# Kernel tuning notes

Measured on AMD Instinct MI355X. Metric: run time of the kernel, lower is better.

Reference implementation:

```python
import math
import jax, jax.numpy as jnp
import numpy as np

D_MODEL = 1024
N_HEAD = 16
HEAD_DIM = D_MODEL // N_HEAD
THETA = 10000.0


def precompute_rope(seq_len, head_dim):
    half = head_dim // 2
    inv_freq = 1.0 / (THETA ** (jnp.arange(half, dtype=jnp.float32) / half))
    pos = jnp.arange(seq_len, dtype=jnp.float32)
    freqs = jnp.outer(pos, inv_freq)  # [S, half]
    return jnp.cos(freqs), jnp.sin(freqs)


def apply_rope(x, cos, sin):
    # x: [B, H, S, Dh]; cos/sin: [S, Dh//2] -> broadcast over B, H
    x_even = x[..., 0::2]
    x_odd = x[..., 1::2]
    cos = cos[None, None]
    sin = sin[None, None]
    out_even = x_even * cos - x_odd * sin
    out_odd = x_even * sin + x_odd * cos
    # interleave back: stack on last axis then flatten pairs
    return jnp.stack((out_even, out_odd), axis=-1).reshape(x.shape)


def setup_inputs() -> dict:
    key = jax.random.key(0)
    kx, kq, kp = jax.random.split(key, 3)
    x = jax.random.normal(kx, (4, 2048, D_MODEL), dtype=jnp.float32)
    s = 1.0 / math.sqrt(D_MODEL)
    # torch Linear weight is [out, in]; we store transposed [in, out] for x @ W
    W_qkv = jax.random.normal(kq, (D_MODEL, 3 * D_MODEL), dtype=jnp.float32) * s
    W_proj = jax.random.normal(kp, (D_MODEL, D_MODEL), dtype=jnp.float32) * s
    return {"x": x, "W_qkv": W_qkv, "W_proj": W_proj}


def reference(x, W_qkv, W_proj):
    bsz, seqlen, d_model = x.shape
    qkv = x @ W_qkv  # [B, S, 3D]
    q, k, v = jnp.split(qkv, 3, axis=-1)
    def to_heads(t):
        return t.reshape(bsz, seqlen, N_HEAD, HEAD_DIM).transpose(0, 2, 1, 3)
    q, k, v = to_heads(q), to_heads(k), to_heads(v)  # [B, H, S, Dh]
    cos, sin = precompute_rope(seqlen, HEAD_DIM)
    q = apply_rope(q, cos, sin)
    k = apply_rope(k, cos, sin)
    att = jnp.einsum('bhqd,bhkd->bhqk', q, k) * (1.0 / math.sqrt(HEAD_DIM))
    causal = jnp.tril(jnp.ones((seqlen, seqlen), dtype=bool))
    att = jnp.where(causal[None, None], att, -jnp.inf)
    att = jax.nn.softmax(att, axis=-1)
    y = jnp.einsum('bhqk,bhkd->bhqd', att, v)
    y = y.transpose(0, 2, 1, 3).reshape(bsz, seqlen, d_model)
    return y @ W_proj
```

## Files before the change

### kernel.cpp

```cpp
#include <hip/hip_runtime.h>


#define BATCH 4
#define SEQ   2048
#define DM    1024
#define NH    16
#define HD    64
#define QKV_W 3072

typedef short bf16x8 __attribute__((ext_vector_type(8)));
typedef float f32x4  __attribute__((ext_vector_type(4)));
typedef unsigned u32x4 __attribute__((ext_vector_type(4)));
typedef unsigned short bf16_t;

__device__ __forceinline__ unsigned short f2bf(float f) {
  unsigned u = __float_as_uint(f);
  u += 0x7fffu + ((u >> 16) & 1u);
  return (unsigned short)(u >> 16);
}
__device__ __forceinline__ float bf2f(unsigned short s) {
  return __uint_as_float((unsigned)s << 16);
}
__device__ __forceinline__ void gld16(const void* g, void* l) {
  __builtin_amdgcn_global_load_lds(
      (const __attribute__((address_space(1))) unsigned int*)g,
      (__attribute__((address_space(3))) unsigned int*)l, 16, 0, 0);
}
__device__ __forceinline__ unsigned cvt_pk_bf16(float a, float b) {
  unsigned r;
  asm("v_cvt_pk_bf16_f32 %0, %1, %2" : "=v"(r) : "v"(a), "v"(b));
  return r;
}
__device__ __forceinline__ void permlane32_swap(unsigned& a, unsigned& b) {
  asm("v_permlane32_swap_b32 %0, %1" : "+v"(a), "+v"(b));
}
__device__ __forceinline__ void permlane16_swap(unsigned& a, unsigned& b) {
  asm("v_permlane16_swap_b32 %0, %1" : "+v"(a), "+v"(b));
}

__global__ __launch_bounds__(256) void k_transpose(const float* __restrict__ W,
                                                   bf16_t* __restrict__ Wt,
                                                   int K, int N) {
  __shared__ float tile[32][33];
  const int tx = threadIdx.x, ty = threadIdx.y;
  const int n0 = blockIdx.x * 32, k0 = blockIdx.y * 32;
#pragma unroll
  for (int j = 0; j < 4; ++j)
    tile[ty + j * 8][tx] = W[(size_t)(k0 + ty + j * 8) * N + n0 + tx];
  __syncthreads();
#pragma unroll
  for (int j = 0; j < 4; ++j)
    Wt[(size_t)(n0 + ty + j * 8) * K + k0 + tx] = f2bf(tile[tx][ty + j * 8]);
}

__global__ __launch_bounds__(256) void k_cvt(const float* __restrict__ x,
                                             bf16_t* __restrict__ xb) {
  const int i = (blockIdx.x * 256 + threadIdx.x) * 4;
  float4 v = *(const float4*)(x + i);
  unsigned lo = (unsigned)f2bf(v.x) | ((unsigned)f2bf(v.y) << 16);
  unsigned hi = (unsigned)f2bf(v.z) | ((unsigned)f2bf(v.w) << 16);
  *(uint2*)(xb + i) = make_uint2(lo, hi);
}

__global__ __launch_bounds__(256) void k_rope(bf16_t* __restrict__ qkv) {
  const int t = blockIdx.x * 256 + threadIdx.x;
  const int i = t & 31;
  const int h = (t >> 5) & 15;
  const int s = (t >> 9) & 2047;
  const int b = t >> 20;
  const float inv = __expf((float)i * -0.28782313662425575f);
  float sn, cs;
  sincosf((float)s * inv, &sn, &cs);
  size_t base = ((size_t)(b * SEQ + s)) * QKV_W + h * HD + 2 * i;
#pragma unroll
  for (int part = 0; part < 2; ++part) {
    unsigned u = *(unsigned*)(qkv + base + part * DM);
    float e = bf2f((unsigned short)(u & 0xffffu));
    float o = bf2f((unsigned short)(u >> 16));
    unsigned short e2 = f2bf(e * cs - o * sn);
    unsigned short o2 = f2bf(e * sn + o * cs);
    *(unsigned*)(qkv + base + part * DM) = (unsigned)e2 | ((unsigned)o2 << 16);
  }
}

template<int MODE>
__global__ __launch_bounds__(256) void k_gemm(const bf16_t* __restrict__ A,
                                              const bf16_t* __restrict__ Bt,
                                              void* __restrict__ Cout,
                                              bf16_t* __restrict__ vt,
                                              int M, int N, int K) {
  __shared__ __align__(16) short As[128 * 64];
  __shared__ __align__(16) short Bs[128 * 64];
  const int tid = threadIdx.x;
  const int wave = tid >> 6, lane = tid & 63;
  const int quad = lane >> 4, l16 = lane & 15;
  const int wm = (wave >> 1) * 64, wn = (wave & 1) * 64;
  const int bm = blockIdx.y * 128, bn = blockIdx.x * 128;

  f32x4 acc[4][4];
#pragma unroll
  for (int i = 0; i < 4; ++i)
#pragma unroll
    for (int j = 0; j < 4; ++j) acc[i][j] = f32x4{0.f, 0.f, 0.f, 0.f};

  const int srow = tid >> 3;
  const int sg   = (tid & 7) ^ (srow & 7);
  const bf16_t* Ap = A  + (size_t)(bm + srow) * K + sg * 8;
  const bf16_t* Bp = Bt + (size_t)(bn + srow) * K + sg * 8;
  short* Ad = As + tid * 8;
  short* Bd = Bs + tid * 8;

  for (int k0 = 0; k0 < K; k0 += 64) {
    __syncthreads();
#pragma unroll
    for (int pp = 0; pp < 4; ++pp) {
      gld16(Ap + (size_t)(pp * 32) * K + k0, Ad + pp * 2048);
      gld16(Bp + (size_t)(pp * 32) * K + k0, Bd + pp * 2048);
    }
    __syncthreads();
#pragma unroll
    for (int ks = 0; ks < 2; ++ks) {
      bf16x8 af[4], bfr[4];
#pragma unroll
      for (int i = 0; i < 4; ++i)
        af[i] = *(const bf16x8*)&As[(wm + i * 16 + l16) * 64 +
                                    (((ks * 4 + quad) ^ (l16 & 7)) << 3)];
#pragma unroll
      for (int j = 0; j < 4; ++j)
        bfr[j] = *(const bf16x8*)&Bs[(wn + j * 16 + l16) * 64 +
                                     (((ks * 4 + quad) ^ (l16 & 7)) << 3)];
#pragma unroll
      for (int i = 0; i < 4; ++i)
#pragma unroll
        for (int j = 0; j < 4; ++j)
          acc[i][j] = __builtin_amdgcn_mfma_f32_16x16x32_bf16(af[i], bfr[j], acc[i][j], 0, 0, 0);
    }
  }
#pragma unroll
  for (int i = 0; i < 4; ++i)
#pragma unroll
    for (int j = 0; j < 4; ++j) {
      const int col = bn + wn + j * 16 + l16;
      const int row0 = bm + wm + i * 16 + quad * 4;
      if (MODE == 1 && col >= 2048) {
        const int d = col - 2048;
        const int hh = d >> 6, dd = d & 63;
        const int bb = row0 >> 11, ss = row0 & 2047;
        ushort4 pk;
        pk.x = f2bf(acc[i][j][0]); pk.y = f2bf(acc[i][j][1]);
        pk.z = f2bf(acc[i][j][2]); pk.w = f2bf(acc[i][j][3]);
        *(ushort4*)(vt + ((size_t)((bb * NH + hh) * HD + dd)) * SEQ + ss) = pk;
      } else {
#pragma unroll
        for (int r = 0; r < 4; ++r) {
          if (MODE == 1)
            ((bf16_t*)Cout)[(size_t)(row0 + r) * N + col] = f2bf(acc[i][j][r]);
          else
            ((float*)Cout)[(size_t)(row0 + r) * N + col] = acc[i][j][r];
        }
      }
    }
}

__global__ __launch_bounds__(512, 2) void k_gqkv(const bf16_t* __restrict__ A,
                                                 const bf16_t* __restrict__ Bt,
                                                 bf16_t* __restrict__ qkv,
                                                 bf16_t* __restrict__ vt) {
  const int K = 1024;
  __shared__ __align__(16) short LA[2 * 2 * 4096];
  __shared__ __align__(16) short LB[2 * 2 * 12288];
  const int tid = threadIdx.x;
  const int lane = tid & 63, wave = tid >> 6;
  const int quad = lane >> 4, l16 = lane & 15;
  const int ah = wave >> 2;
  const int wn4 = wave & 3;

  int bid = (int)blockIdx.x;
  bid = (bid & 7) * 64 + (bid >> 3);
  const int bm = (bid >> 3) * 128, bn = (bid & 7) * 384;

  f32x4 acc[4][6];
#pragma unroll
  for (int i = 0; i < 4; ++i)
#pragma unroll
    for (int j = 0; j < 6; ++j) acc[i][j] = f32x4{0.f, 0.f, 0.f, 0.f};

  const int sg = (tid & 3) ^ ((tid >> 2) & 3) ^ ((tid >> 4) & 3);
  const bf16_t* aS = A  + (size_t)(bm + (tid >> 2)) * K + sg * 8;
  const bf16_t* bS = Bt + (size_t)(bn + (tid >> 2)) * K + sg * 8;
  short* dA = LA + tid * 8;
  short* dB = LB + tid * 8;

  const int g = quad ^ (l16 & 3) ^ ((l16 >> 2) & 3);
  const int abase = (ah * 64 + l16) * 32 + g * 8;
  const int bbase = (wn4 * 96 + l16) * 32 + g * 8;

#define WAITV(n) asm volatile("s_waitcnt vmcnt(" n ")" ::: "memory")
#define STGR(kts, kss)                                                         \
  do {                                                                         \
    const size_t kc_ = (size_t)((kts) * 64 + (kss) * 32);                      \
    const int rb_ = ((kts) & 1) * 2 + (kss);                                   \
    gld16(aS + kc_, dA + rb_ * 4096);                                          \
    gld16(bS + kc_, dB + rb_ * 12288);                                         \
    gld16(bS + (size_t)128 * 1024 + kc_, dB + rb_ * 12288 + 4096);             \
    gld16(bS + (size_t)256 * 1024 + kc_, dB + rb_ * 12288 + 8192);             \
  } while (0)
#define PHASE(kt, ks, STAGE_STMT, WAIT_STMT)                                   \
  do {                                                                         \
    const short* la_ = LA + (((kt) & 1) * 2 + (ks)) * 4096 + abase;            \
    const short* lb_ = LB + (((kt) & 1) * 2 + (ks)) * 12288 + bbase;           \
    bf16x8 af[4], bfr[6];                                                      \
    _Pragma("unroll") for (int mi = 0; mi < 4; ++mi)                           \
        af[mi] = *(const bf16x8*)(la_ + mi * 512);                             \
    _Pragma("unroll") for (int nj = 0; nj < 6; ++nj)                           \
        bfr[nj] = *(const bf16x8*)(lb_ + nj * 512);                            \
    STAGE_STMT;                                                                \
    WAIT_STMT;                                                                 \
    __builtin_amdgcn_s_barrier();                                              \
    __builtin_amdgcn_s_setprio(1);                                             \
    _Pragma("unroll") for (int mi = 0; mi < 4; ++mi)                           \
      _Pragma("unroll") for (int nj = 0; nj < 6; ++nj)                         \
        acc[mi][nj] = __builtin_amdgcn_mfma_f32_16x16x32_bf16(                 \
            af[mi], bfr[nj], acc[mi][nj], 0, 0, 0);                            \
    __builtin_amdgcn_s_setprio(0);                                             \
    asm volatile("s_waitcnt lgkmcnt(0)" ::: "memory");                         \
    __builtin_amdgcn_s_barrier();                                              \
  } while (0)

  STGR(0, 0); STGR(0, 1); STGR(1, 0);
  WAITV("8");
  __builtin_amdgcn_s_barrier();

#pragma unroll 1
  for (int ph = 0; ph < 29; ++ph) {
    const int kt = ph >> 1, ks = ph & 1;
    const int pk = ph + 3;
    PHASE(kt, ks, STGR(pk >> 1, pk & 1), WAITV("8"));
  }
  PHASE(14, 1, (void)0, WAITV("4"));
  PHASE(15, 0, (void)0, WAITV("0"));
  PHASE(15, 1, (void)0, (void)0);

#pragma unroll
  for (int mi = 0; mi < 4; ++mi)
#pragma unroll
    for (int nj = 0; nj < 6; ++nj) {
      const int col = bn + wn4 * 96 + nj * 16 + l16;
      const int row0 = bm + ah * 64 + mi * 16 + quad * 4;
      if (col >= 2048) {
        const int d = col - 2048;
        const int hh = d >> 6, dd = d & 63;
        const int bb = row0 >> 11, ss = row0 & 2047;
        ushort4 pk;
        pk.x = f2bf(acc[mi][nj][0]); pk.y = f2bf(acc[mi][nj][1]);
        pk.z = f2bf(acc[mi][nj][2]); pk.w = f2bf(acc[mi][nj][3]);
        *(ushort4*)(vt + ((size_t)((bb * NH + hh) * HD + dd)) * SEQ + ss) = pk;
      } else {
#pragma unroll
        for (int r = 0; r < 4; ++r)
          qkv[(size_t)(row0 + r) * QKV_W + col] = f2bf(acc[mi][nj][r]);
      }
    }
#undef WAITV
#undef STGR
#undef PHASE
}

#define QSCALE 0.18033688011112042f
__global__ __launch_bounds__(256, 2) void k_attn(const bf16_t* __restrict__ qkv,
                                                 const bf16_t* __restrict__ vt,
                                                 bf16_t* __restrict__ y) {
  __shared__ __align__(16) short KV[2][4][64 * 32];
  const int tid = threadIdx.x;
  const int lane = tid & 63;
  const int quad = lane >> 4, l16 = lane & 15;
  const int wave = tid >> 6;
  const int l = blockIdx.x;
  const int p = (l >> 3) & 7;
  const int g = ((l >> 6) << 3) | (l & 7);
  const int h = g & 15, b = g >> 4;
  const size_t bbase = (size_t)b * SEQ * QKV_W;
  const int srow = tid >> 2;
  const int sc8  = (tid & 3) * 8;
  const bf16_t* kbase = qkv + bbase + (size_t)srow * QKV_W + DM + h * HD + sc8;
  const bf16_t* vbase = vt + ((size_t)(b * NH + h) * HD + srow) * SEQ + sc8;

#define ISSUE(kv0, buf)                                              \
  do {                                                               \
    gld16(kbase + (size_t)(kv0) * QKV_W,      &KV[buf][0][tid * 8]); \
    gld16(kbase + (size_t)(kv0) * QKV_W + 32, &KV[buf][1][tid * 8]); \
    gld16(vbase + (kv0),                      &KV[buf][2][tid * 8]); \
    gld16(vbase + (kv0) + 32,                 &KV[buf][3][tid * 8]); \
  } while (0)

  int bufp = 0;
  ISSUE(0, 0);
  for (int half = 0; half < 2; ++half) {
    const int qt = half ? (15 - p) : p;
    const int qb = qt * 128 + wave * 32;
    bf16x8 aq[2][2];
#pragma unroll
    for (int mi = 0; mi < 2; ++mi)
#pragma unroll
      for (int kk = 0; kk < 2; ++kk) {
        const bf16_t* qp = qkv + bbase + (size_t)(qb + mi * 16 + l16) * QKV_W +
                           h * HD + kk * 32 + quad * 8;
        bf16x8 raw = *(const bf16x8*)qp;
        bf16x8 sc;
#pragma unroll
        for (int e = 0; e < 8; ++e)
          sc[e] = (short)f2bf(bf2f((unsigned short)raw[e]) * QSCALE);
        aq[mi][kk] = sc;
      }
    f32x4 o[2][4];
    float lsum[2];
#pragma unroll
    for (int mi = 0; mi < 2; ++mi) {
      lsum[mi] = 0.f;
#pragma unroll
      for (int jn = 0; jn < 4; ++jn) o[mi][jn] = f32x4{0.f, 0.f, 0.f, 0.f};
    }
    const int qr0 = qb + l16;

    const int jmax = 2 * qt + 1;
    for (int j = 0; j <= jmax; ++j) {
      const int kv0 = j * 64;
      __syncthreads();
      if (j < jmax)          ISSUE(kv0 + 64, bufp ^ 1);
      else if (half == 0)    ISSUE(0, bufp ^ 1);
      if (kv0 <= qb + 31) {
        const bool needmask = (kv0 + 63 > qb);
        const short* Kc0 = &KV[bufp][0][0];
        const short* Kc1 = &KV[bufp][1][0];
        const short* Vc0 = &KV[bufp][2][0];
        const short* Vc1 = &KV[bufp][3][0];

        f32x4 st[4][2];
#pragma unroll
        for (int jn = 0; jn < 4; ++jn) {
          bf16x8 ak0 = *(const bf16x8*)&Kc0[(jn * 16 + l16) * 32 + quad * 8];
          bf16x8 ak1 = *(const bf16x8*)&Kc1[(jn * 16 + l16) * 32 + quad * 8];
#pragma unroll
          for (int mi = 0; mi < 2; ++mi) {
            f32x4 s4 = f32x4{0.f, 0.f, 0.f, 0.f};
            s4 = __builtin_amdgcn_mfma_f32_16x16x32_bf16(ak0, aq[mi][0], s4, 0, 0, 0);
            s4 = __builtin_amdgcn_mfma_f32_16x16x32_bf16(ak1, aq[mi][1], s4, 0, 0, 0);
            st[jn][mi] = s4;
          }
        }
        unsigned pk[4][2][2];
#pragma unroll
        for (int jn = 0; jn < 4; ++jn)
#pragma unroll
          for (int mi = 0; mi < 2; ++mi) {
            const int kvb = kv0 + jn * 16 + quad * 4;
            const int qr = qr0 + mi * 16;
            float e[4];
#pragma unroll
            for (int r = 0; r < 4; ++r) {
              float v = __builtin_amdgcn_exp2f(st[jn][mi][r]);
              if (needmask) v = (kvb + r <= qr) ? v : 0.f;
              lsum[mi] += v;
              e[r] = v;
            }
            pk[jn][mi][0] = cvt_pk_bf16(e[0], e[1]);
            pk[jn][mi][1] = cvt_pk_bf16(e[2], e[3]);
          }
        bf16x8 ap[2][2];
#pragma unroll
        for (int mi = 0; mi < 2; ++mi)
#pragma unroll
          for (int ks = 0; ks < 2; ++ks) {
            unsigned a0 = pk[2 * ks][mi][0], b0 = pk[2 * ks + 1][mi][0];
            permlane32_swap(a0, b0);
            permlane16_swap(a0, b0);
            unsigned a1 = pk[2 * ks][mi][1], b1 = pk[2 * ks + 1][mi][1];
            permlane32_swap(a1, b1);
            permlane16_swap(a1, b1);
            union { u32x4 u; bf16x8 s; } f;
            f.u = (u32x4){a0, a1, b0, b1};
            ap[mi][ks] = f.s;
          }
#pragma unroll
        for (int ks = 0; ks < 2; ++ks) {
          const short* Vc = ks ? Vc1 : Vc0;
#pragma unroll
          for (int jn = 0; jn < 4; ++jn) {
            bf16x8 bv = *(const bf16x8*)&Vc[(jn * 16 + l16) * 32 + quad * 8];
            o[0][jn] = __builtin_amdgcn_mfma_f32_16x16x32_bf16(ap[0][ks], bv, o[0][jn], 0, 0, 0);
            o[1][jn] = __builtin_amdgcn_mfma_f32_16x16x32_bf16(ap[1][ks], bv, o[1][jn], 0, 0, 0);
          }
        }
      }
      bufp ^= 1;
    }
#pragma unroll
    for (int mi = 0; mi < 2; ++mi) {
      float s = lsum[mi];
      s += __shfl_xor(s, 16, 64);
      s += __shfl_xor(s, 32, 64);
      const float inv = 1.0f / s;
#pragma unroll
      for (int r = 0; r < 4; ++r) {
        const float invr = __shfl(inv, quad * 4 + r, 64);
        const int qr = qb + mi * 16 + quad * 4 + r;
        bf16_t* yp = y + ((size_t)b * SEQ + qr) * DM + h * HD;
#pragma unroll
        for (int jn = 0; jn < 4; ++jn)
          yp[jn * 16 + l16] = f2bf(o[mi][jn][r] * invr);
      }
    }
  }
#undef ISSUE
}

extern "C" void kernel_launch(void* const* d_in, const int* in_sizes, int n_in,
                              void* d_out, int out_size, void* d_ws, size_t ws_size,
                              hipStream_t stream) {
  const float* x     = (const float*)d_in[0];
  const float* Wqkv  = (const float*)d_in[1];
  const float* Wproj = (const float*)d_in[2];
  float* out = (float*)d_out;
  char* ws = (char*)d_ws;
  bf16_t* qkv = (bf16_t*)(ws);
  bf16_t* Wt1 = (bf16_t*)(ws + 50331648);
  bf16_t* Wt2 = (bf16_t*)(ws + 56623104);
  bf16_t* xb  = (bf16_t*)(ws + 58720256);
  bf16_t* y   = xb;
  bf16_t* vt  = (bf16_t*)d_out;

  k_transpose<<<dim3(QKV_W / 32, DM / 32), dim3(32, 8), 0, stream>>>(Wqkv, Wt1, DM, QKV_W);
  k_transpose<<<dim3(DM / 32, DM / 32), dim3(32, 8), 0, stream>>>(Wproj, Wt2, DM, DM);
  k_cvt<<<(BATCH * SEQ * DM) / (4 * 256), 256, 0, stream>>>(x, xb);
  k_gqkv<<<512, 512, 0, stream>>>(xb, Wt1, qkv, vt);
  k_rope<<<(BATCH * SEQ * NH * 32) / 256, 256, 0, stream>>>(qkv);
  k_attn<<<512, 256, 0, stream>>>(qkv, vt, y);
  k_gemm<0><<<dim3(DM / 128, (BATCH * SEQ) / 128), 256, 0, stream>>>(
      y, Wt2, out, nullptr, BATCH * SEQ, DM, DM);
}
```

Before: 258.8 us.

## Restructure QKV GEMM to double-buffered 64-wide K tiles with split staging

Reworks the QKV projection GEMM main loop. The old version ran a 4-slot ring of 32-wide K slices with two barriers per half-step; the new one uses two buffers of 64-wide K tiles with an XOR swizzle over 8 slots. Global-to-LDS loads for the next tile are issued in two halves, interleaved between the two MFMA sub-steps, so there are fewer barriers per K iteration. The trade-off is shallower prefetch depth (one tile ahead instead of three slices), which could expose more memory latency.

```diff
diff --git a/kernel.cpp b/kernel.cpp
--- a/kernel.cpp
+++ b/kernel.cpp
@@ -167,17 +167,17 @@
                                                  bf16_t* __restrict__ qkv,
                                                  bf16_t* __restrict__ vt) {
   const int K = 1024;
-  __shared__ __align__(16) short LA[2 * 2 * 4096];
-  __shared__ __align__(16) short LB[2 * 2 * 12288];
+  __shared__ __align__(16) short LA[2][128 * 64];
+  __shared__ __align__(16) short LB[2][384 * 64];
   const int tid = threadIdx.x;
   const int lane = tid & 63, wave = tid >> 6;
   const int quad = lane >> 4, l16 = lane & 15;
   const int ah = wave >> 2;
   const int wn4 = wave & 3;
 
-  int bid = (int)blockIdx.x;
-  bid = (bid & 7) * 64 + (bid >> 3);
-  const int bm = (bid >> 3) * 128, bn = (bid & 7) * 384;
+  const int b0 = (int)blockIdx.x;
+  const int wg = (b0 & 7) * 64 + (b0 >> 3);
+  const int bm = (wg >> 3) * 128, bn = (wg & 7) * 384;
 
   f32x4 acc[4][6];
 #pragma unroll
@@ -185,61 +185,76 @@
 #pragma unroll
     for (int j = 0; j < 6; ++j) acc[i][j] = f32x4{0.f, 0.f, 0.f, 0.f};
 
-  const int sg = (tid & 3) ^ ((tid >> 2) & 3) ^ ((tid >> 4) & 3);
-  const bf16_t* aS = A  + (size_t)(bm + (tid >> 2)) * K + sg * 8;
-  const bf16_t* bS = Bt + (size_t)(bn + (tid >> 2)) * K + sg * 8;
-  short* dA = LA + tid * 8;
-  short* dB = LB + tid * 8;
-
-  const int g = quad ^ (l16 & 3) ^ ((l16 >> 2) & 3);
-  const int abase = (ah * 64 + l16) * 32 + g * 8;
-  const int bbase = (wn4 * 96 + l16) * 32 + g * 8;
-
-#define WAITV(n) asm volatile("s_waitcnt vmcnt(" n ")" ::: "memory")
-#define STGR(kts, kss)                                                         \
+  const int srow = tid >> 3;
+  const int sg   = (tid & 7) ^ (srow & 7);
+  const bf16_t* aS = A  + (size_t)(bm + srow) * K + sg * 8;
+  const bf16_t* bS = Bt + (size_t)(bn + srow) * K + sg * 8;
+
+  const int arow = ah * 64 + l16;
+  const int brow = wn4 * 96 + l16;
+  const int xs = l16 & 7;
+
+#define STGA(buf, n, kt) \
+  gld16(aS + (size_t)((n) * 64) * K + (kt) * 64, &LA[buf][(n) * 4096 + tid * 8])
+#define STGB(buf, n, kt) \
+  gld16(bS + (size_t)((n) * 64) * K + (kt) * 64, &LB[buf][(n) * 4096 + tid * 8])
+#define STG03(buf, kt) \
+  do { STGA(buf, 0, kt); STGA(buf, 1, kt); STGB(buf, 0, kt); STGB(buf, 1, kt); } while (0)
+#define STG47(buf, kt) \
+  do { STGB(buf, 2, kt); STGB(buf, 3, kt); STGB(buf, 4, kt); STGB(buf, 5, kt); } while (0)
+#define READS(buf, ks, af, bfr)                                                \
   do {                                                                         \
-    const size_t kc_ = (size_t)((kts) * 64 + (kss) * 32);                      \
-    const int rb_ = ((kts) & 1) * 2 + (kss);                                   \
-    gld16(aS + kc_, dA + rb_ * 4096);                                          \
-    gld16(bS + kc_, dB + rb_ * 12288);                                         \
-    gld16(bS + (size_t)128 * 1024 + kc_, dB + rb_ * 12288 + 4096);             \
-    gld16(bS + (size_t)256 * 1024 + kc_, dB + rb_ * 12288 + 8192);             \
+    const int slot_ = ((((ks) * 4 + quad) ^ xs) << 3);                         \
+    _Pragma("unroll") for (int mi = 0; mi < 4; ++mi)                           \
+        af[mi] = *(const bf16x8*)&LA[buf][(arow + mi * 16) * 64 + slot_];      \
+    _Pragma("unroll") for (int nj = 0; nj < 6; ++nj)                           \
+        bfr[nj] = *(const bf16x8*)&LB[buf][(brow + nj * 16) * 64 + slot_];     \
   } while (0)
-#define PHASE(kt, ks, STAGE_STMT, WAIT_STMT)                                   \
+#define MFMAS(af, bfr)                                                         \
   do {                                                                         \
-    const short* la_ = LA + (((kt) & 1) * 2 + (ks)) * 4096 + abase;            \
-    const short* lb_ = LB + (((kt) & 1) * 2 + (ks)) * 12288 + bbase;           \
-    bf16x8 af[4], bfr[6];                                                      \
-    _Pragma("unroll") for (int mi = 0; mi < 4; ++mi)                           \
-        af[mi] = *(const bf16x8*)(la_ + mi * 512);                             \
-    _Pragma("unroll") for (int nj = 0; nj < 6; ++nj)                           \
-        bfr[nj] = *(const bf16x8*)(lb_ + nj * 512);                            \
-    STAGE_STMT;                                                                \
-    WAIT_STMT;                                                                 \
-    __builtin_amdgcn_s_barrier();                                              \
     __builtin_amdgcn_s_setprio(1);                                             \
     _Pragma("unroll") for (int mi = 0; mi < 4; ++mi)                           \
       _Pragma("unroll") for (int nj = 0; nj < 6; ++nj)                         \
         acc[mi][nj] = __builtin_amdgcn_mfma_f32_16x16x32_bf16(                 \
             af[mi], bfr[nj], acc[mi][nj], 0, 0, 0);                            \
     __builtin_amdgcn_s_setprio(0);                                             \
-    asm volatile("s_waitcnt lgkmcnt(0)" ::: "memory");                         \
-    __builtin_amdgcn_s_barrier();                                              \
   } while (0)
 
-  STGR(0, 0); STGR(0, 1); STGR(1, 0);
-  WAITV("8");
+  STG03(0, 0); STG47(0, 0);
+
+#pragma unroll 1
+  for (int kt = 0; kt < 15; ++kt) {
+    const int cb = kt & 1, nb = cb ^ 1;
+    STG03(nb, kt + 1);
+    asm volatile("s_waitcnt vmcnt(4)" ::: "memory");
+    __builtin_amdgcn_s_barrier();
+    asm volatile("" ::: "memory");
+    {
+      bf16x8 af[4], bfr[6];
+      READS(cb, 0, af, bfr);
+      MFMAS(af, bfr);
+    }
+    STG47(nb, kt + 1);
+    {
+      bf16x8 af[4], bfr[6];
+      READS(cb, 1, af, bfr);
+      MFMAS(af, bfr);
+    }
+    __builtin_amdgcn_s_barrier();
+  }
+  asm volatile("s_waitcnt vmcnt(0)" ::: "memory");
   __builtin_amdgcn_s_barrier();
-
-#pragma unroll 1
-  for (int ph = 0; ph < 29; ++ph) {
-    const int kt = ph >> 1, ks = ph & 1;
-    const int pk = ph + 3;
-    PHASE(kt, ks, STGR(pk >> 1, pk & 1), WAITV("8"));
-  }
-  PHASE(14, 1, (void)0, WAITV("4"));
-  PHASE(15, 0, (void)0, WAITV("0"));
-  PHASE(15, 1, (void)0, (void)0);
+  asm volatile("" ::: "memory");
+  {
+    bf16x8 af[4], bfr[6];
+    READS(1, 0, af, bfr);
+    MFMAS(af, bfr);
+  }
+  {
+    bf16x8 af[4], bfr[6];
+    READS(1, 1, af, bfr);
+    MFMAS(af, bfr);
+  }
 
 #pragma unroll
   for (int mi = 0; mi < 4; ++mi)
@@ -261,9 +276,12 @@
           qkv[(size_t)(row0 + r) * QKV_W + col] = f2bf(acc[mi][nj][r]);
       }
     }
-#undef WAITV
-#undef STGR
-#undef PHASE
+#undef STGA
+#undef STGB
+#undef STG03
+#undef STG47
+#undef READS
+#undef MFMAS
 }
 
 #define QSCALE 0.18033688011112042f
```

Result: faster. 252.3 us (-2.5%).
